# Kernel optimization log

Measured on AMD Instinct MI355X. Metric: run time of the kernel, lower is better.

Reference implementation:

```python
import jax, jax.numpy as jnp
import numpy as np

# SLAYER neuron / simulation constants (from netParams yaml)
THETA = 10.0      # spike threshold
TAU_SR = 10.0     # PSP (SRM) time constant, ms
TS = 1.0          # simulation time step, ms
TAU_RHO = 1.0     # surrogate-gradient width
SCALE_RHO = 1.0   # surrogate-gradient scale
N_TIME_BINS = 300 # tSample / Ts


@jax.custom_vjp
def spike_fn(u):
    # Hard threshold forward; surrogate gradient backward (SLAYER escape-rate pdf).
    return (u >= THETA).astype(u.dtype)

def _spike_fwd(u):
    return spike_fn(u), u

def _spike_bwd(u, g):
    return (g * SCALE_RHO * jnp.exp(-jnp.abs(u - THETA) / TAU_RHO),)

spike_fn.defvjp(_spike_fwd, _spike_bwd)


def psp(x):
    # Causal leaky-integrator (first-order SRM) filter over time.
    # x: [B, T, F] -> u[t] = decay * u[t-1] + x[t]
    decay = jnp.exp(jnp.asarray(-TS / TAU_SR, x.dtype))
    xT = jnp.swapaxes(x, 0, 1)  # [T, B, F]
    def step(u, xt):
        u = decay * u + xt
        return u, u
    _, out = jax.lax.scan(step, jnp.zeros_like(xT[0]), xT)
    return jnp.swapaxes(out, 0, 1)  # [B, T, F]


def rate_encode(inp, n_time_bins, key):
    # Bernoulli rate coding: spike prob per time bin = pixel intensity in [0,1].
    # inp: [B, C, H, W] -> spikes: [B, T, C*H*W]
    B = inp.shape[0]
    probs = inp.reshape(B, 1, -1)  # [B, 1, F]
    u = jax.random.uniform(key, (B, n_time_bins, probs.shape[-1]), dtype=inp.dtype)
    return (u < probs).astype(inp.dtype)


def setup_inputs() -> dict:
    key = jax.random.key(0)
    k1, k2, k3 = jax.random.split(key, 3)
    B, C, H, W = 32, 3, 32, 32
    F_in, F_hid, F_out = C * H * W, 410, 10
    inp = jax.random.uniform(k1, (B, C, H, W), dtype=jnp.float32)
    W1 = jax.random.normal(k2, (F_hid, F_in), dtype=jnp.float32) / np.sqrt(F_in).astype(np.float32)
    W2 = jax.random.normal(k3, (F_out, F_hid), dtype=jnp.float32) / np.sqrt(F_hid).astype(np.float32)
    return {"inp": inp, "W1": W1, "W2": W2}


def reference(inp, W1, W2):
    spikes = rate_encode(inp, N_TIME_BINS, jax.random.key(42))   # [B, T, 3072]
    a1 = jnp.einsum('btf,of->bto', spikes, W1)                    # dense per time bin
    s1 = spike_fn(psp(a1))                                        # [B, T, 410]
    a2 = jnp.einsum('btf,of->bto', s1, W2)
    s2 = spike_fn(psp(a2))                                        # [B, T, 10]
    return jnp.swapaxes(s2, 1, 2)                                 # [B, 10, T]
```

## Files before the change

### kernel.cpp

```cpp
#include <hip/hip_runtime.h>
#include <stdint.h>

#define B_SZ 32
#define T_SZ 300
#define F_IN 3072
#define F_HID 410
#define F_OUT 10
#define M_SZ (B_SZ * T_SZ)
#define N_PAD 448
#define A2_STRIDE 16
#define SB2_STRIDE 16
#define NCHUNK 10
#define CLEN 30
#define NKB (F_IN / 256)
#define MT_CNT (M_SZ / 64)
#define W1_BLOCKS 672
#define RNG_BLOCKS 14400

#define DECAY 0.90483741803595957f
#define THETA 10.0f
#define KS2 (0x1BD11BDAu ^ 42u)

typedef __attribute__((ext_vector_type(8))) int i32x8;
typedef __attribute__((ext_vector_type(16))) float f32x16;

#define TF_R(r) { x0 += x1; \
  asm("v_alignbit_b32 %0, %0, %0, %1" : "+v"(x1) : "n"(32 - (r))); \
  x1 ^= x0; }

__device__ __forceinline__ uint32_t tf_bits(uint32_t x1i) {
  uint32_t x0 = 0u, x1 = x1i;
  TF_R(13) TF_R(15) TF_R(26) TF_R(6)
  x0 += 42u; x1 += KS2 + 1u;
  TF_R(17) TF_R(29) TF_R(16) TF_R(24)
  x0 += KS2; x1 += 2u;
  TF_R(13) TF_R(15) TF_R(26) TF_R(6)
  x1 += 42u + 3u;
  TF_R(17) TF_R(29) TF_R(16) TF_R(24)
  x0 += 42u; x1 += KS2 + 4u;
  TF_R(13) TF_R(15) TF_R(26) TF_R(6)
  x0 += KS2; x1 += 5u;
  return x0 ^ x1;
}

__device__ __forceinline__ void gld16(const void* g, void* l) {
  __builtin_amdgcn_global_load_lds(
      (const __attribute__((address_space(1))) uint32_t*)g,
      (__attribute__((address_space(3))) uint32_t*)l, 16, 0, 0);
}

__global__ __launch_bounds__(256) void prep(const float* __restrict__ inp,
                                            const float* __restrict__ W1,
                                            uint8_t* __restrict__ W1s,
                                            uint32_t* __restrict__ sbitsT) {
  if (blockIdx.x < W1_BLOCKS) {
    int idx = blockIdx.x * 256 + threadIdx.x;
    int g = idx * 8;
    int n = g / F_IN;
    int k = g - n * F_IN;
    uint32_t d0 = 0u, d1 = 0u;
    if (n < F_HID) {
      const float* s = W1 + (size_t)n * F_IN + k;
      float4 v0 = ((const float4*)s)[0];
      float4 v1 = ((const float4*)s)[1];
      int t0 = __builtin_amdgcn_cvt_pk_fp8_f32(v0.x, v0.y, 0, false);
      t0 = __builtin_amdgcn_cvt_pk_fp8_f32(v0.z, v0.w, t0, true);
      int t1 = __builtin_amdgcn_cvt_pk_fp8_f32(v1.x, v1.y, 0, false);
      t1 = __builtin_amdgcn_cvt_pk_fp8_f32(v1.z, v1.w, t1, true);
      d0 = (uint32_t)t0; d1 = (uint32_t)t1;
    }
    int nt = n >> 6, r = n & 63;
    int kb = k >> 8, c = (k >> 4) & 15, half = (k >> 3) & 1;
    size_t dst = ((((size_t)nt * NKB + kb) * 64 + r) * 16 + (c ^ (r & 15))) * 16 + half * 8;
    *(uint2*)(W1s + dst) = make_uint2(d0, d1);
  } else {
    uint32_t idx = (blockIdx.x - W1_BLOCKS) * 256u + threadIdx.x;
    uint32_t q = idx & 3u;
    uint32_t j = idx >> 2;
    uint32_t r = j & 63u;
    uint32_t t1 = j >> 6;
    uint32_t wi = t1 & 7u;
    uint32_t t2 = t1 >> 3;
    uint32_t kb = t2 % (uint32_t)NKB;
    uint32_t mt = t2 / (uint32_t)NKB;
    uint32_t m = mt * 64u + r;
    uint32_t b = m / (uint32_t)T_SZ;
    uint32_t f = (kb * 8u + wi) * 32u + q * 8u;
    const float* p = inp + b * F_IN + f;
    float4 va = ((const float4*)p)[0];
    float4 vb = ((const float4*)p)[1];
    uint32_t T0 = (uint32_t)ceilf(va.x * 8388608.0f);
    uint32_t T1 = (uint32_t)ceilf(va.y * 8388608.0f);
    uint32_t T2 = (uint32_t)ceilf(va.z * 8388608.0f);
    uint32_t T3 = (uint32_t)ceilf(va.w * 8388608.0f);
    uint32_t T4 = (uint32_t)ceilf(vb.x * 8388608.0f);
    uint32_t T5 = (uint32_t)ceilf(vb.y * 8388608.0f);
    uint32_t T6 = (uint32_t)ceilf(vb.z * 8388608.0f);
    uint32_t T7 = (uint32_t)ceilf(vb.w * 8388608.0f);
    uint32_t b42 = m * (uint32_t)F_IN + f + 42u;
    uint32_t w = 0u;
#define GEN(jj, Tn) { uint32_t bits = tf_bits(b42 + (jj)); \
  w |= ((bits >> 9) < (Tn)) ? (1u << (jj)) : 0u; }
    GEN(0, T0) GEN(1, T1) GEN(2, T2) GEN(3, T3)
    GEN(4, T4) GEN(5, T5) GEN(6, T6) GEN(7, T7)
#undef GEN
    ((uint8_t*)sbitsT)[idx] = (uint8_t)w;
  }
}

__global__ __launch_bounds__(256) void gemm1(const uint32_t* __restrict__ sbitsT,
                                             const uint8_t* __restrict__ W1s,
                                             float* __restrict__ a1) {
  __shared__ uint32_t sAT[2][8 * 64];
  __shared__ uint8_t sB[2][64 * 256];

  const int tid = threadIdx.x;
  const int mtile = blockIdx.x;
  const int nt = blockIdx.y;
  const int m0 = mtile * 64;
  const int n0 = nt * 64;
  const int wv = tid >> 6, lane = tid & 63;
  const int wm = (wv & 1) * 32, wn = (wv >> 1) * 32;
  const int l31 = lane & 31, lh = lane >> 5;

  const uint8_t* gB0 = W1s + (size_t)nt * NKB * 16384;
  const uint8_t* gA0 = (const uint8_t*)sbitsT + (size_t)mtile * NKB * 2048;

  auto STAGE = [&](int buf, int kb) {
    const uint8_t* gB = gB0 + (size_t)kb * 16384;
#pragma unroll
    for (int q = 0; q < 4; ++q)
      gld16(gB + (wv * 4 + q) * 1024 + lane * 16, &sB[buf][(wv * 4 + q) * 1024]);
    if (wv < 2)
      gld16(gA0 + (size_t)kb * 2048 + wv * 1024 + lane * 16,
            (uint8_t*)&sAT[buf][0] + wv * 1024);
  };

  f32x16 acc;
#pragma unroll
  for (int e = 0; e < 16; ++e) acc[e] = 0.0f;

  STAGE(0, 0);
  __syncthreads();
  int cur = 0;
  for (int kb = 0; kb < NKB; ++kb) {
    if (kb + 1 < NKB) STAGE(cur ^ 1, kb + 1);
    const uint8_t* sBc = sB[cur];
    const uint32_t* sATc = sAT[cur];
#pragma unroll
    for (int sub = 0; sub < 4; ++sub) {
      int row = wn + l31;
      int cb = sub * 4 + lh * 2;
      uint4 u0 = *(uint4*)&sBc[row * 256 + (((cb + 0) ^ (row & 15)) << 4)];
      uint4 u1 = *(uint4*)&sBc[row * 256 + (((cb + 1) ^ (row & 15)) << 4)];
      i32x8 bfr;
      bfr[0] = u0.x; bfr[1] = u0.y; bfr[2] = u0.z; bfr[3] = u0.w;
      bfr[4] = u1.x; bfr[5] = u1.y; bfr[6] = u1.z; bfr[7] = u1.w;
      uint32_t w = sATc[(sub * 2 + lh) * 64 + wm + l31];
      i32x8 afr;
#pragma unroll
      for (int j = 0; j < 8; ++j) {
        uint32_t n = (w >> (4 * j)) & 15u;
        afr[j] = (int)(((n * 0x204081u) & 0x01010101u) * 0x38u);
      }
      acc = __builtin_amdgcn_mfma_scale_f32_32x32x64_f8f6f4(
          afr, bfr, acc, 0, 0, 0, 127, 0, 127);
    }
    __syncthreads();
    cur ^= 1;
  }
  int col = n0 + wn + l31;
#pragma unroll
  for (int rg = 0; rg < 16; ++rg) {
    int row = m0 + wm + (rg & 3) + 8 * (rg >> 2) + 4 * lh;
    a1[(size_t)row * N_PAD + col] = acc[rg];
  }
}

__global__ __launch_bounds__(640) void scan_spike(const float* __restrict__ a1,
                                                  uint32_t* __restrict__ sb2) {
  __shared__ float fin_s[NCHUNK][64];
  const int oblk = blockIdx.x;
  const int b = blockIdx.y;
  const int c = threadIdx.x >> 6;
  const int lane = threadIdx.x & 63;
  const int o = oblk * 64 + lane;
  const float* p = a1 + ((size_t)(b * T_SZ + c * CLEN)) * N_PAD + o;
  float pa[CLEN];
  float u = 0.0f;
#pragma unroll
  for (int i = 0; i < CLEN; ++i) {
    u = __fadd_rn(__fmul_rn(DECAY, u), p[(size_t)i * N_PAD]);
    pa[i] = u;
  }
  fin_s[c][lane] = u;
  __syncthreads();
  float d30 = 1.0f;
#pragma unroll
  for (int i = 0; i < CLEN; ++i) d30 *= DECAY;
  float F = 0.0f;
  for (int cc = 0; cc < c; ++cc)
    F = fin_s[cc][lane] + d30 * F;
  float dp = DECAY;
  const int m0 = b * T_SZ + c * CLEN;
#pragma unroll
  for (int i = 0; i < CLEN; ++i) {
    float uu = (c > 0) ? __fadd_rn(pa[i], __fmul_rn(dp, F)) : pa[i];
    unsigned long long msk = __ballot(uu >= THETA);
    if (lane == 0)
      *(uint2*)&sb2[(size_t)(m0 + i) * SB2_STRIDE + oblk * 2] =
          make_uint2((uint32_t)msk, (uint32_t)(msk >> 32));
    dp *= DECAY;
  }
}

__global__ __launch_bounds__(256) void gemm2(const uint32_t* __restrict__ sb2,
                                             const float* __restrict__ W2,
                                             float* __restrict__ a2) {
  __shared__ float sW2[F_OUT * F_HID];
  for (int i = threadIdx.x; i < F_OUT * F_HID; i += 256) sW2[i] = W2[i];
  __syncthreads();
  int m = blockIdx.x * 4 + (threadIdx.x >> 6);
  int lane = threadIdx.x & 63;
  int lh = lane >> 5;
  float p[F_OUT];
#pragma unroll
  for (int o = 0; o < F_OUT; ++o) p[o] = 0.0f;
#pragma unroll
  for (int j = 0; j < 7; ++j) {
    int hh = lane + j * 64;
    uint32_t w = sb2[(size_t)m * SB2_STRIDE + j * 2 + lh];
    float s = (float)((w >> (lane & 31)) & 1u);
    int hcl = hh < F_HID ? hh : 0;
#pragma unroll
    for (int o = 0; o < F_OUT; ++o) p[o] = fmaf(s, sW2[o * F_HID + hcl], p[o]);
  }
#pragma unroll
  for (int o = 0; o < F_OUT; ++o)
#pragma unroll
    for (int s = 1; s < 64; s <<= 1) p[o] += __shfl_xor(p[o], s, 64);
  if (lane < F_OUT) a2[(size_t)m * A2_STRIDE + lane] = p[lane];
}

__global__ __launch_bounds__(128) void psp2(const float* __restrict__ a2,
                                            float* __restrict__ out) {
  __shared__ float chf[NCHUNK][F_OUT];
  __shared__ float seed[NCHUNK][F_OUT];
  int b = blockIdx.x;
  int tid = threadIdx.x;
  int o = tid / NCHUNK, c = tid % NCHUNK;
  const float* p = a2 + ((size_t)(b * T_SZ + c * CLEN)) * A2_STRIDE + o;
  float v[CLEN];
  float pa[CLEN];
  if (tid < F_OUT * NCHUNK) {
#pragma unroll
    for (int i = 0; i < CLEN; ++i) v[i] = p[(size_t)i * A2_STRIDE];
    float u = 0.0f;
#pragma unroll
    for (int i = 0; i < CLEN; ++i) {
      u = __fadd_rn(__fmul_rn(DECAY, u), v[i]);
      pa[i] = u;
    }
    chf[c][o] = u;
  }
  __syncthreads();
  if (tid < F_OUT) {
    float d30 = 1.0f;
#pragma unroll
    for (int i = 0; i < CLEN; ++i) d30 *= DECAY;
    float F = 0.0f;
    for (int cc = 0; cc < NCHUNK; ++cc) {
      F = chf[cc][tid] + d30 * F;
      seed[cc][tid] = F;
    }
  }
  __syncthreads();
  if (tid < F_OUT * NCHUNK) {
    float F = (c == 0) ? 0.0f : seed[c - 1][o];
    float dp = DECAY;
    float* q = out + (size_t)b * F_OUT * T_SZ + (size_t)o * T_SZ + c * CLEN;
#pragma unroll
    for (int i = 0; i < CLEN; ++i) {
      float u = (c == 0) ? pa[i] : __fadd_rn(pa[i], __fmul_rn(dp, F));
      q[i] = (u >= THETA) ? 1.0f : 0.0f;
      dp *= DECAY;
    }
  }
}

extern "C" void kernel_launch(void* const* d_in, const int* in_sizes, int n_in,
                              void* d_out, int out_size, void* d_ws, size_t ws_size,
                              hipStream_t stream) {
  const float* inp = (const float*)d_in[0];
  const float* W1  = (const float*)d_in[1];
  const float* W2  = (const float*)d_in[2];
  float* out = (float*)d_out;
  char* ws = (char*)d_ws;
  uint8_t* W1s = (uint8_t*)(ws);
  uint32_t* sbitsT = (uint32_t*)(ws + 1376256);
  float* a1 = (float*)(ws + 1376256 + 3686400);
  uint32_t* sb2 = (uint32_t*)((char*)a1 + (size_t)M_SZ * N_PAD * 4);
  float* a2 = (float*)((char*)sb2 + (size_t)M_SZ * SB2_STRIDE * 4);

  prep<<<dim3(W1_BLOCKS + RNG_BLOCKS), dim3(256), 0, stream>>>(inp, W1, W1s, sbitsT);
  gemm1<<<dim3(MT_CNT, N_PAD / 64), dim3(256), 0, stream>>>(sbitsT, W1s, a1);
  scan_spike<<<dim3(N_PAD / 64, B_SZ), dim3(640), 0, stream>>>(a1, sb2);
  gemm2<<<dim3(M_SZ / 4), dim3(256), 0, stream>>>(sb2, W2, a2);
  psp2<<<dim3(B_SZ), dim3(128), 0, stream>>>(a2, out);
}
```

Measured before the change: 161.0 us.

## Fuse hidden-layer scan, second GEMM and output PSP into one per-batch kernel

Replaces three kernels (scan_spike, gemm2, psp2) with a single layer2 kernel that runs one 1024-thread block per batch element. Spike bits and layer-2 activations stay in shared memory instead of going through global workspace, which removes two launches and the intermediate global traffic. In exchange a1 is read twice (once for chunk finals, once to recompute the scan), and only 32 blocks run, so parallelism across the GPU is much lower than in the old 3-kernel split.

```diff
diff --git a/kernel.cpp b/kernel.cpp
--- a/kernel.cpp
+++ b/kernel.cpp
@@ -8,8 +8,6 @@
 #define F_OUT 10
 #define M_SZ (B_SZ * T_SZ)
 #define N_PAD 448
-#define A2_STRIDE 16
-#define SB2_STRIDE 16
 #define NCHUNK 10
 #define CLEN 30
 #define NKB (F_IN / 256)
@@ -177,113 +175,128 @@
   }
 }
 
-__global__ __launch_bounds__(640) void scan_spike(const float* __restrict__ a1,
-                                                  uint32_t* __restrict__ sb2) {
-  __shared__ float fin_s[NCHUNK][64];
-  const int oblk = blockIdx.x;
-  const int b = blockIdx.y;
-  const int c = threadIdx.x >> 6;
-  const int lane = threadIdx.x & 63;
-  const int o = oblk * 64 + lane;
-  const float* p = a1 + ((size_t)(b * T_SZ + c * CLEN)) * N_PAD + o;
-  float pa[CLEN];
-  float u = 0.0f;
-#pragma unroll
-  for (int i = 0; i < CLEN; ++i) {
-    u = __fadd_rn(__fmul_rn(DECAY, u), p[(size_t)i * N_PAD]);
-    pa[i] = u;
-  }
-  fin_s[c][lane] = u;
-  __syncthreads();
-  float d30 = 1.0f;
-#pragma unroll
-  for (int i = 0; i < CLEN; ++i) d30 *= DECAY;
-  float F = 0.0f;
-  for (int cc = 0; cc < c; ++cc)
-    F = fin_s[cc][lane] + d30 * F;
-  float dp = DECAY;
-  const int m0 = b * T_SZ + c * CLEN;
-#pragma unroll
-  for (int i = 0; i < CLEN; ++i) {
-    float uu = (c > 0) ? __fadd_rn(pa[i], __fmul_rn(dp, F)) : pa[i];
-    unsigned long long msk = __ballot(uu >= THETA);
-    if (lane == 0)
-      *(uint2*)&sb2[(size_t)(m0 + i) * SB2_STRIDE + oblk * 2] =
-          make_uint2((uint32_t)msk, (uint32_t)(msk >> 32));
-    dp *= DECAY;
-  }
-}
-
-__global__ __launch_bounds__(256) void gemm2(const uint32_t* __restrict__ sb2,
-                                             const float* __restrict__ W2,
-                                             float* __restrict__ a2) {
+__global__ __launch_bounds__(1024) void layer2(const float* __restrict__ a1,
+                                               const float* __restrict__ W2,
+                                               float* __restrict__ out) {
   __shared__ float sW2[F_OUT * F_HID];
-  for (int i = threadIdx.x; i < F_OUT * F_HID; i += 256) sW2[i] = W2[i];
-  __syncthreads();
-  int m = blockIdx.x * 4 + (threadIdx.x >> 6);
-  int lane = threadIdx.x & 63;
-  int lh = lane >> 5;
-  float p[F_OUT];
-#pragma unroll
-  for (int o = 0; o < F_OUT; ++o) p[o] = 0.0f;
-#pragma unroll
-  for (int j = 0; j < 7; ++j) {
-    int hh = lane + j * 64;
-    uint32_t w = sb2[(size_t)m * SB2_STRIDE + j * 2 + lh];
-    float s = (float)((w >> (lane & 31)) & 1u);
-    int hcl = hh < F_HID ? hh : 0;
-#pragma unroll
-    for (int o = 0; o < F_OUT; ++o) p[o] = fmaf(s, sW2[o * F_HID + hcl], p[o]);
-  }
-#pragma unroll
-  for (int o = 0; o < F_OUT; ++o)
-#pragma unroll
-    for (int s = 1; s < 64; s <<= 1) p[o] += __shfl_xor(p[o], s, 64);
-  if (lane < F_OUT) a2[(size_t)m * A2_STRIDE + lane] = p[lane];
-}
-
-__global__ __launch_bounds__(128) void psp2(const float* __restrict__ a2,
-                                            float* __restrict__ out) {
+  __shared__ float finF[NCHUNK][N_PAD];
+  __shared__ uint32_t sbits[T_SZ][14];
+  __shared__ float a2s[T_SZ][F_OUT];
   __shared__ float chf[NCHUNK][F_OUT];
   __shared__ float seed[NCHUNK][F_OUT];
-  int b = blockIdx.x;
-  int tid = threadIdx.x;
-  int o = tid / NCHUNK, c = tid % NCHUNK;
-  const float* p = a2 + ((size_t)(b * T_SZ + c * CLEN)) * A2_STRIDE + o;
-  float v[CLEN];
-  float pa[CLEN];
-  if (tid < F_OUT * NCHUNK) {
-#pragma unroll
-    for (int i = 0; i < CLEN; ++i) v[i] = p[(size_t)i * A2_STRIDE];
+  const int b = blockIdx.x;
+  const int tid = threadIdx.x;
+  const int w = tid >> 6, lane = tid & 63;
+
+  for (int i = tid; i < F_OUT * F_HID; i += 1024) sW2[i] = W2[i];
+
+  for (int p = w; p < NCHUNK * 7; p += 16) {
+    int c = p / 7, ob = p % 7;
+    const float* src = a1 + ((size_t)(b * T_SZ + c * CLEN)) * N_PAD + ob * 64 + lane;
     float u = 0.0f;
 #pragma unroll
-    for (int i = 0; i < CLEN; ++i) {
-      u = __fadd_rn(__fmul_rn(DECAY, u), v[i]);
-      pa[i] = u;
-    }
-    chf[c][o] = u;
-  }
-  __syncthreads();
-  if (tid < F_OUT) {
+    for (int i = 0; i < CLEN; ++i)
+      u = __fadd_rn(__fmul_rn(DECAY, u), src[(size_t)i * N_PAD]);
+    finF[c][ob * 64 + lane] = u;
+  }
+  __syncthreads();
+
+  if (tid < N_PAD) {
+    float v[NCHUNK];
+#pragma unroll
+    for (int c = 0; c < NCHUNK; ++c) v[c] = finF[c][tid];
     float d30 = 1.0f;
 #pragma unroll
     for (int i = 0; i < CLEN; ++i) d30 *= DECAY;
     float F = 0.0f;
-    for (int cc = 0; cc < NCHUNK; ++cc) {
-      F = chf[cc][tid] + d30 * F;
-      seed[cc][tid] = F;
-    }
-  }
-  __syncthreads();
-  if (tid < F_OUT * NCHUNK) {
-    float F = (c == 0) ? 0.0f : seed[c - 1][o];
+    finF[0][tid] = 0.0f;
+#pragma unroll
+    for (int c = 1; c < NCHUNK; ++c) {
+      F = v[c - 1] + d30 * F;
+      finF[c][tid] = F;
+    }
+  }
+  __syncthreads();
+
+  for (int p = w; p < NCHUNK * 7; p += 16) {
+    int c = p / 7, ob = p % 7;
+    const float* src = a1 + ((size_t)(b * T_SZ + c * CLEN)) * N_PAD + ob * 64 + lane;
+    float F = finF[c][ob * 64 + lane];
+    float u = 0.0f;
     float dp = DECAY;
-    float* q = out + (size_t)b * F_OUT * T_SZ + (size_t)o * T_SZ + c * CLEN;
+    int m0 = c * CLEN;
 #pragma unroll
     for (int i = 0; i < CLEN; ++i) {
-      float u = (c == 0) ? pa[i] : __fadd_rn(pa[i], __fmul_rn(dp, F));
-      q[i] = (u >= THETA) ? 1.0f : 0.0f;
+      u = __fadd_rn(__fmul_rn(DECAY, u), src[(size_t)i * N_PAD]);
+      float uu = (c > 0) ? __fadd_rn(u, __fmul_rn(dp, F)) : u;
+      unsigned long long msk = __ballot(uu >= THETA);
+      if (lane == 0)
+        *(uint2*)&sbits[m0 + i][ob * 2] =
+            make_uint2((uint32_t)msk, (uint32_t)(msk >> 32));
       dp *= DECAY;
+    }
+  }
+  __syncthreads();
+
+  for (int m = w; m < T_SZ; m += 16) {
+    int lh = lane >> 5;
+    float p[F_OUT];
+#pragma unroll
+    for (int o = 0; o < F_OUT; ++o) p[o] = 0.0f;
+#pragma unroll
+    for (int j = 0; j < 7; ++j) {
+      int hh = lane + j * 64;
+      uint32_t wd = sbits[m][j * 2 + lh];
+      float s = (float)((wd >> (lane & 31)) & 1u);
+      int hcl = hh < F_HID ? hh : 0;
+#pragma unroll
+      for (int o = 0; o < F_OUT; ++o) p[o] = fmaf(s, sW2[o * F_HID + hcl], p[o]);
+    }
+#pragma unroll
+    for (int o = 0; o < F_OUT; ++o)
+#pragma unroll
+      for (int s2 = 1; s2 < 64; s2 <<= 1) p[o] += __shfl_xor(p[o], s2, 64);
+    if (lane < F_OUT) a2s[m][lane] = p[lane];
+  }
+  __syncthreads();
+
+  {
+    int o = tid / NCHUNK, c = tid % NCHUNK;
+    float v[CLEN];
+    float pa[CLEN];
+    if (tid < F_OUT * NCHUNK) {
+#pragma unroll
+      for (int i = 0; i < CLEN; ++i) v[i] = a2s[c * CLEN + i][o];
+      float u = 0.0f;
+#pragma unroll
+      for (int i = 0; i < CLEN; ++i) {
+        u = __fadd_rn(__fmul_rn(DECAY, u), v[i]);
+        pa[i] = u;
+      }
+      chf[c][o] = u;
+    }
+    __syncthreads();
+    if (tid < F_OUT) {
+      float d30 = 1.0f;
+#pragma unroll
+      for (int i = 0; i < CLEN; ++i) d30 *= DECAY;
+      float F = 0.0f;
+      for (int cc = 0; cc < NCHUNK; ++cc) {
+        F = chf[cc][tid] + d30 * F;
+        seed[cc][tid] = F;
+      }
+    }
+    __syncthreads();
+    if (tid < F_OUT * NCHUNK) {
+      float F = (c == 0) ? 0.0f : seed[c - 1][o];
+      float dp = DECAY;
+      float* q = out + (size_t)b * F_OUT * T_SZ + (size_t)o * T_SZ + c * CLEN;
+#pragma unroll
+      for (int i = 0; i < CLEN; ++i) {
+        float u = (c == 0) ? pa[i] : __fadd_rn(pa[i], __fmul_rn(dp, F));
+        q[i] = (u >= THETA) ? 1.0f : 0.0f;
+        dp *= DECAY;
+      }
     }
   }
 }
@@ -299,12 +312,8 @@
   uint8_t* W1s = (uint8_t*)(ws);
   uint32_t* sbitsT = (uint32_t*)(ws + 1376256);
   float* a1 = (float*)(ws + 1376256 + 3686400);
-  uint32_t* sb2 = (uint32_t*)((char*)a1 + (size_t)M_SZ * N_PAD * 4);
-  float* a2 = (float*)((char*)sb2 + (size_t)M_SZ * SB2_STRIDE * 4);
 
   prep<<<dim3(W1_BLOCKS + RNG_BLOCKS), dim3(256), 0, stream>>>(inp, W1, W1s, sbitsT);
   gemm1<<<dim3(MT_CNT, N_PAD / 64), dim3(256), 0, stream>>>(sbitsT, W1s, a1);
-  scan_spike<<<dim3(N_PAD / 64, B_SZ), dim3(640), 0, stream>>>(a1, sb2);
-  gemm2<<<dim3(M_SZ / 4), dim3(256), 0, stream>>>(sb2, W2, a2);
-  psp2<<<dim3(B_SZ), dim3(128), 0, stream>>>(a2, out);
-}
+  layer2<<<dim3(B_SZ), dim3(1024), 0, stream>>>(a1, W2, out);
+}
```

Result: slower. 216.8 us (+34.6%).

## Fuse prep and GEMM1 into one kernel with atomic-counter dataflow waits

Applied to the files above, without the earlier changes.

Merges the W1 fp8 conversion / RNG spike-encoding kernel and the first GEMM into a single launch. GEMM tiles spin on per-m-tile and W1 completion counters, which are zeroed by a tiny extra kernel and stored in padding slots of the a2 buffer. This lets GEMM work start as soon as its inputs are ready, overlapping it with RNG generation and removing a kernel boundary. In exchange, the GEMM drops LDS double buffering to single buffering, and it relies on blocks being dispatched in index order to avoid deadlock.

```diff
diff --git a/kernel.cpp b/kernel.cpp
--- a/kernel.cpp
+++ b/kernel.cpp
@@ -16,6 +16,8 @@
 #define MT_CNT (M_SZ / 64)
 #define W1_BLOCKS 672
 #define RNG_BLOCKS 14400
+#define GEMM_BLOCKS (MT_CNT * (N_PAD / 64))
+#define PG1_BLOCKS (W1_BLOCKS + RNG_BLOCKS + GEMM_BLOCKS)
 
 #define DECAY 0.90483741803595957f
 #define THETA 10.0f
@@ -49,12 +51,25 @@
       (__attribute__((address_space(3))) uint32_t*)l, 16, 0, 0);
 }
 
-__global__ __launch_bounds__(256) void prep(const float* __restrict__ inp,
-                                            const float* __restrict__ W1,
-                                            uint8_t* __restrict__ W1s,
-                                            uint32_t* __restrict__ sbitsT) {
-  if (blockIdx.x < W1_BLOCKS) {
-    int idx = blockIdx.x * 256 + threadIdx.x;
+__device__ __forceinline__ uint32_t* ctr_slot(uint32_t* ctr, int i) {
+  return ctr + (size_t)i * A2_STRIDE + 10;
+}
+
+__global__ __launch_bounds__(256) void zeroctr(uint32_t* __restrict__ ctr) {
+  if (threadIdx.x < 152) *ctr_slot(ctr, threadIdx.x) = 0u;
+}
+
+__global__ __launch_bounds__(256, 5) void pg1(
+    const float* __restrict__ inp, const float* __restrict__ W1,
+    uint8_t* __restrict__ W1s, uint32_t* __restrict__ sbitsT,
+    float* __restrict__ a1, uint32_t* __restrict__ ctr) {
+  __shared__ uint32_t sAT[8 * 64];
+  __shared__ uint8_t sB[64 * 256];
+  const int tid = threadIdx.x;
+  const int bid = blockIdx.x;
+
+  if (bid < W1_BLOCKS) {
+    int idx = bid * 256 + tid;
     int g = idx * 8;
     int n = g / F_IN;
     int k = g - n * F_IN;
@@ -73,8 +88,11 @@
     int kb = k >> 8, c = (k >> 4) & 15, half = (k >> 3) & 1;
     size_t dst = ((((size_t)nt * NKB + kb) * 64 + r) * 16 + (c ^ (r & 15))) * 16 + half * 8;
     *(uint2*)(W1s + dst) = make_uint2(d0, d1);
-  } else {
-    uint32_t idx = (blockIdx.x - W1_BLOCKS) * 256u + threadIdx.x;
+    __syncthreads();
+    if (tid == 0) { __threadfence(); atomicAdd(ctr_slot(ctr, 1), 1u); }
+  } else if (bid < W1_BLOCKS + RNG_BLOCKS) {
+    uint32_t bp = bid - W1_BLOCKS;
+    uint32_t idx = bp * 256u + tid;
     uint32_t q = idx & 3u;
     uint32_t j = idx >> 2;
     uint32_t r = j & 63u;
@@ -105,75 +123,72 @@
     GEN(4, T4) GEN(5, T5) GEN(6, T6) GEN(7, T7)
 #undef GEN
     ((uint8_t*)sbitsT)[idx] = (uint8_t)w;
-  }
-}
-
-__global__ __launch_bounds__(256) void gemm1(const uint32_t* __restrict__ sbitsT,
-                                             const uint8_t* __restrict__ W1s,
-                                             float* __restrict__ a1) {
-  __shared__ uint32_t sAT[2][8 * 64];
-  __shared__ uint8_t sB[2][64 * 256];
-
-  const int tid = threadIdx.x;
-  const int mtile = blockIdx.x;
-  const int nt = blockIdx.y;
-  const int m0 = mtile * 64;
-  const int n0 = nt * 64;
-  const int wv = tid >> 6, lane = tid & 63;
-  const int wm = (wv & 1) * 32, wn = (wv >> 1) * 32;
-  const int l31 = lane & 31, lh = lane >> 5;
-
-  const uint8_t* gB0 = W1s + (size_t)nt * NKB * 16384;
-  const uint8_t* gA0 = (const uint8_t*)sbitsT + (size_t)mtile * NKB * 2048;
-
-  auto STAGE = [&](int buf, int kb) {
-    const uint8_t* gB = gB0 + (size_t)kb * 16384;
-#pragma unroll
-    for (int q = 0; q < 4; ++q)
-      gld16(gB + (wv * 4 + q) * 1024 + lane * 16, &sB[buf][(wv * 4 + q) * 1024]);
-    if (wv < 2)
-      gld16(gA0 + (size_t)kb * 2048 + wv * 1024 + lane * 16,
-            (uint8_t*)&sAT[buf][0] + wv * 1024);
-  };
-
-  f32x16 acc;
-#pragma unroll
-  for (int e = 0; e < 16; ++e) acc[e] = 0.0f;
-
-  STAGE(0, 0);
-  __syncthreads();
-  int cur = 0;
-  for (int kb = 0; kb < NKB; ++kb) {
-    if (kb + 1 < NKB) STAGE(cur ^ 1, kb + 1);
-    const uint8_t* sBc = sB[cur];
-    const uint32_t* sATc = sAT[cur];
-#pragma unroll
-    for (int sub = 0; sub < 4; ++sub) {
-      int row = wn + l31;
-      int cb = sub * 4 + lh * 2;
-      uint4 u0 = *(uint4*)&sBc[row * 256 + (((cb + 0) ^ (row & 15)) << 4)];
-      uint4 u1 = *(uint4*)&sBc[row * 256 + (((cb + 1) ^ (row & 15)) << 4)];
-      i32x8 bfr;
-      bfr[0] = u0.x; bfr[1] = u0.y; bfr[2] = u0.z; bfr[3] = u0.w;
-      bfr[4] = u1.x; bfr[5] = u1.y; bfr[6] = u1.z; bfr[7] = u1.w;
-      uint32_t w = sATc[(sub * 2 + lh) * 64 + wm + l31];
-      i32x8 afr;
-#pragma unroll
-      for (int j = 0; j < 8; ++j) {
-        uint32_t n = (w >> (4 * j)) & 15u;
-        afr[j] = (int)(((n * 0x204081u) & 0x01010101u) * 0x38u);
+    __syncthreads();
+    if (tid == 0) { __threadfence(); atomicAdd(ctr_slot(ctr, 2 + bp / 96), 1u); }
+  } else {
+    int g = bid - (W1_BLOCKS + RNG_BLOCKS);
+    const int mtile = g % MT_CNT;
+    const int nt = g / MT_CNT;
+    if (tid == 0) {
+      while (__hip_atomic_load(ctr_slot(ctr, 2 + mtile), __ATOMIC_RELAXED,
+                               __HIP_MEMORY_SCOPE_AGENT) < 96u)
+        __builtin_amdgcn_s_sleep(4);
+      while (__hip_atomic_load(ctr_slot(ctr, 1), __ATOMIC_RELAXED,
+                               __HIP_MEMORY_SCOPE_AGENT) < (uint32_t)W1_BLOCKS)
+        __builtin_amdgcn_s_sleep(4);
+      __threadfence();
+    }
+    __syncthreads();
+
+    const int m0 = mtile * 64;
+    const int n0 = nt * 64;
+    const int wv = tid >> 6, lane = tid & 63;
+    const int wm = (wv & 1) * 32, wn = (wv >> 1) * 32;
+    const int l31 = lane & 31, lh = lane >> 5;
+
+    const uint8_t* gB0 = W1s + (size_t)nt * NKB * 16384;
+    const uint8_t* gA0 = (const uint8_t*)sbitsT + (size_t)mtile * NKB * 2048;
+
+    f32x16 acc;
+#pragma unroll
+    for (int e = 0; e < 16; ++e) acc[e] = 0.0f;
+
+    for (int kb = 0; kb < NKB; ++kb) {
+      const uint8_t* gB = gB0 + (size_t)kb * 16384;
+#pragma unroll
+      for (int q = 0; q < 4; ++q)
+        gld16(gB + (wv * 4 + q) * 1024 + lane * 16, &sB[(wv * 4 + q) * 1024]);
+      if (wv < 2)
+        gld16(gA0 + (size_t)kb * 2048 + wv * 1024 + lane * 16,
+              (uint8_t*)sAT + wv * 1024);
+      __syncthreads();
+#pragma unroll
+      for (int sub = 0; sub < 4; ++sub) {
+        int row = wn + l31;
+        int cb = sub * 4 + lh * 2;
+        uint4 u0 = *(uint4*)&sB[row * 256 + (((cb + 0) ^ (row & 15)) << 4)];
+        uint4 u1 = *(uint4*)&sB[row * 256 + (((cb + 1) ^ (row & 15)) << 4)];
+        i32x8 bfr;
+        bfr[0] = u0.x; bfr[1] = u0.y; bfr[2] = u0.z; bfr[3] = u0.w;
+        bfr[4] = u1.x; bfr[5] = u1.y; bfr[6] = u1.z; bfr[7] = u1.w;
+        uint32_t w = sAT[(sub * 2 + lh) * 64 + wm + l31];
+        i32x8 afr;
+#pragma unroll
+        for (int j = 0; j < 8; ++j) {
+          uint32_t n = (w >> (4 * j)) & 15u;
+          afr[j] = (int)(((n * 0x204081u) & 0x01010101u) * 0x38u);
+        }
+        acc = __builtin_amdgcn_mfma_scale_f32_32x32x64_f8f6f4(
+            afr, bfr, acc, 0, 0, 0, 127, 0, 127);
       }
-      acc = __builtin_amdgcn_mfma_scale_f32_32x32x64_f8f6f4(
-          afr, bfr, acc, 0, 0, 0, 127, 0, 127);
-    }
-    __syncthreads();
-    cur ^= 1;
-  }
-  int col = n0 + wn + l31;
-#pragma unroll
-  for (int rg = 0; rg < 16; ++rg) {
-    int row = m0 + wm + (rg & 3) + 8 * (rg >> 2) + 4 * lh;
-    a1[(size_t)row * N_PAD + col] = acc[rg];
+      __syncthreads();
+    }
+    int col = n0 + wn + l31;
+#pragma unroll
+    for (int rg = 0; rg < 16; ++rg) {
+      int row = m0 + wm + (rg & 3) + 8 * (rg >> 2) + 4 * lh;
+      a1[(size_t)row * N_PAD + col] = acc[rg];
+    }
   }
 }
 
@@ -301,9 +316,10 @@
   float* a1 = (float*)(ws + 1376256 + 3686400);
   uint32_t* sb2 = (uint32_t*)((char*)a1 + (size_t)M_SZ * N_PAD * 4);
   float* a2 = (float*)((char*)sb2 + (size_t)M_SZ * SB2_STRIDE * 4);
-
-  prep<<<dim3(W1_BLOCKS + RNG_BLOCKS), dim3(256), 0, stream>>>(inp, W1, W1s, sbitsT);
-  gemm1<<<dim3(MT_CNT, N_PAD / 64), dim3(256), 0, stream>>>(sbitsT, W1s, a1);
+  uint32_t* ctr = (uint32_t*)a2;
+
+  zeroctr<<<dim3(1), dim3(256), 0, stream>>>(ctr);
+  pg1<<<dim3(PG1_BLOCKS), dim3(256), 0, stream>>>(inp, W1, W1s, sbitsT, a1, ctr);
   scan_spike<<<dim3(N_PAD / 64, B_SZ), dim3(640), 0, stream>>>(a1, sb2);
   gemm2<<<dim3(M_SZ / 4), dim3(256), 0, stream>>>(sb2, W2, a2);
   psp2<<<dim3(B_SZ), dim3(128), 0, stream>>>(a2, out);
```

Measured after the change: 377.1 us. 2.34x slower.

## Enlarge gemm1 block tile to 128 rows with two accumulators per wave

Applied to the files above, without the earlier changes.

The gemm1 block tile grows from 64x64 to 128x64. Each wave now covers 32 rows across all 64 columns and keeps two MFMA accumulators, so every expanded A fragment is reused for two MFMAs. This halves the number of blocks and the W1 tile reloads per M row, and adds nontemporal stores for the a1 output. The cost is more registers per wave and fewer blocks in the grid, which can lower occupancy and latency hiding.

```diff
diff --git a/kernel.cpp b/kernel.cpp
--- a/kernel.cpp
+++ b/kernel.cpp
@@ -14,6 +14,7 @@
 #define CLEN 30
 #define NKB (F_IN / 256)
 #define MT_CNT (M_SZ / 64)
+#define MT2 (M_SZ / 128)
 #define W1_BLOCKS 672
 #define RNG_BLOCKS 14400
 
@@ -111,34 +112,35 @@
 __global__ __launch_bounds__(256) void gemm1(const uint32_t* __restrict__ sbitsT,
                                              const uint8_t* __restrict__ W1s,
                                              float* __restrict__ a1) {
-  __shared__ uint32_t sAT[2][8 * 64];
+  __shared__ uint32_t sAT[2][2][512];
   __shared__ uint8_t sB[2][64 * 256];
 
   const int tid = threadIdx.x;
-  const int mtile = blockIdx.x;
+  const int bx = blockIdx.x;
   const int nt = blockIdx.y;
-  const int m0 = mtile * 64;
+  const int m0 = bx * 128;
   const int n0 = nt * 64;
   const int wv = tid >> 6, lane = tid & 63;
-  const int wm = (wv & 1) * 32, wn = (wv >> 1) * 32;
+  const int wm = wv * 32;
+  const int half = wv >> 1;
+  const int lrow = (wv & 1) * 32;
   const int l31 = lane & 31, lh = lane >> 5;
 
   const uint8_t* gB0 = W1s + (size_t)nt * NKB * 16384;
-  const uint8_t* gA0 = (const uint8_t*)sbitsT + (size_t)mtile * NKB * 2048;
+  const uint8_t* gA0 = (const uint8_t*)sbitsT + (size_t)(2 * bx) * NKB * 2048;
 
   auto STAGE = [&](int buf, int kb) {
     const uint8_t* gB = gB0 + (size_t)kb * 16384;
 #pragma unroll
     for (int q = 0; q < 4; ++q)
       gld16(gB + (wv * 4 + q) * 1024 + lane * 16, &sB[buf][(wv * 4 + q) * 1024]);
-    if (wv < 2)
-      gld16(gA0 + (size_t)kb * 2048 + wv * 1024 + lane * 16,
-            (uint8_t*)&sAT[buf][0] + wv * 1024);
+    gld16(gA0 + (size_t)half * NKB * 2048 + (size_t)kb * 2048 + (wv & 1) * 1024 + lane * 16,
+          (uint8_t*)&sAT[buf][half][0] + (wv & 1) * 1024);
   };
 
-  f32x16 acc;
-#pragma unroll
-  for (int e = 0; e < 16; ++e) acc[e] = 0.0f;
+  f32x16 acc0, acc1;
+#pragma unroll
+  for (int e = 0; e < 16; ++e) { acc0[e] = 0.0f; acc1[e] = 0.0f; }
 
   STAGE(0, 0);
   __syncthreads();
@@ -146,34 +148,40 @@
   for (int kb = 0; kb < NKB; ++kb) {
     if (kb + 1 < NKB) STAGE(cur ^ 1, kb + 1);
     const uint8_t* sBc = sB[cur];
-    const uint32_t* sATc = sAT[cur];
+    const uint32_t* sATc = &sAT[cur][half][0];
 #pragma unroll
     for (int sub = 0; sub < 4; ++sub) {
-      int row = wn + l31;
       int cb = sub * 4 + lh * 2;
-      uint4 u0 = *(uint4*)&sBc[row * 256 + (((cb + 0) ^ (row & 15)) << 4)];
-      uint4 u1 = *(uint4*)&sBc[row * 256 + (((cb + 1) ^ (row & 15)) << 4)];
-      i32x8 bfr;
-      bfr[0] = u0.x; bfr[1] = u0.y; bfr[2] = u0.z; bfr[3] = u0.w;
-      bfr[4] = u1.x; bfr[5] = u1.y; bfr[6] = u1.z; bfr[7] = u1.w;
-      uint32_t w = sATc[(sub * 2 + lh) * 64 + wm + l31];
+      int r0 = l31, r1 = 32 + l31;
+      uint4 a0 = *(uint4*)&sBc[r0 * 256 + (((cb + 0) ^ (r0 & 15)) << 4)];
+      uint4 a1v = *(uint4*)&sBc[r0 * 256 + (((cb + 1) ^ (r0 & 15)) << 4)];
+      uint4 b0 = *(uint4*)&sBc[r1 * 256 + (((cb + 0) ^ (r1 & 15)) << 4)];
+      uint4 b1 = *(uint4*)&sBc[r1 * 256 + (((cb + 1) ^ (r1 & 15)) << 4)];
+      i32x8 bfr0, bfr1;
+      bfr0[0] = a0.x; bfr0[1] = a0.y; bfr0[2] = a0.z; bfr0[3] = a0.w;
+      bfr0[4] = a1v.x; bfr0[5] = a1v.y; bfr0[6] = a1v.z; bfr0[7] = a1v.w;
+      bfr1[0] = b0.x; bfr1[1] = b0.y; bfr1[2] = b0.z; bfr1[3] = b0.w;
+      bfr1[4] = b1.x; bfr1[5] = b1.y; bfr1[6] = b1.z; bfr1[7] = b1.w;
+      uint32_t w = sATc[(sub * 2 + lh) * 64 + lrow + l31];
       i32x8 afr;
 #pragma unroll
       for (int j = 0; j < 8; ++j) {
         uint32_t n = (w >> (4 * j)) & 15u;
         afr[j] = (int)(((n * 0x204081u) & 0x01010101u) * 0x38u);
       }
-      acc = __builtin_amdgcn_mfma_scale_f32_32x32x64_f8f6f4(
-          afr, bfr, acc, 0, 0, 0, 127, 0, 127);
+      acc0 = __builtin_amdgcn_mfma_scale_f32_32x32x64_f8f6f4(
+          afr, bfr0, acc0, 0, 0, 0, 127, 0, 127);
+      acc1 = __builtin_amdgcn_mfma_scale_f32_32x32x64_f8f6f4(
+          afr, bfr1, acc1, 0, 0, 0, 127, 0, 127);
     }
     __syncthreads();
     cur ^= 1;
   }
-  int col = n0 + wn + l31;
 #pragma unroll
   for (int rg = 0; rg < 16; ++rg) {
     int row = m0 + wm + (rg & 3) + 8 * (rg >> 2) + 4 * lh;
-    a1[(size_t)row * N_PAD + col] = acc[rg];
+    __builtin_nontemporal_store(acc0[rg], &a1[(size_t)row * N_PAD + n0 + l31]);
+    __builtin_nontemporal_store(acc1[rg], &a1[(size_t)row * N_PAD + n0 + 32 + l31]);
   }
 }
 
@@ -303,7 +311,7 @@
   float* a2 = (float*)((char*)sb2 + (size_t)M_SZ * SB2_STRIDE * 4);
 
   prep<<<dim3(W1_BLOCKS + RNG_BLOCKS), dim3(256), 0, stream>>>(inp, W1, W1s, sbitsT);
-  gemm1<<<dim3(MT_CNT, N_PAD / 64), dim3(256), 0, stream>>>(sbitsT, W1s, a1);
+  gemm1<<<dim3(MT2, N_PAD / 64), dim3(256), 0, stream>>>(sbitsT, W1s, a1);
   scan_spike<<<dim3(N_PAD / 64, B_SZ), dim3(640), 0, stream>>>(a1, sb2);
   gemm2<<<dim3(M_SZ / 4), dim3(256), 0, stream>>>(sb2, W2, a2);
   psp2<<<dim3(B_SZ), dim3(128), 0, stream>>>(a2, out);
```

Result: faster. 155.4 us (-3.5%).
